# Optimization experiments

Hardware: AMD Instinct MI355X
Metric: run time of the kernel (lower is better)

Reference implementation:

```python
import jax, jax.numpy as jnp
import numpy as np
import math

B, N, H, D = 2, 2048, 16, 64

def setup_inputs() -> dict:
    key = jax.random.key(0)
    kq, kk, kv = jax.random.split(key, 3)
    q = jax.random.normal(kq, (B, N, H, D), dtype=jnp.float32)
    k = jax.random.normal(kk, (B, N, H, D), dtype=jnp.float32)
    v = jax.random.normal(kv, (B, N, H, D), dtype=jnp.float32)
    return {"q": q, "k": k, "v": v}

def reference(q, k, v):
    d = q.shape[-1]
    # [b,n,h,d] -> [b,h,n,d]
    qh = jnp.transpose(q, (0, 2, 1, 3))
    kh = jnp.transpose(k, (0, 2, 1, 3))
    vh = jnp.transpose(v, (0, 2, 1, 3))
    # scores: [b,h,n,n]
    scores = jnp.einsum('bhqd,bhkd->bhqk', qh, kh) / math.sqrt(d)
    # jax.nn.softmax performs the stable max-subtraction internally,
    # matching the original's explicit max-subtract + softmax.
    attn = jax.nn.softmax(scores, axis=-1)
    o = jnp.einsum('bhqk,bhkd->bhqd', attn, vh)
    # back to [b,n,h,d]
    return jnp.transpose(o, (0, 2, 1, 3))
```

## Files before the change

kernel.cpp:

```cpp
#include <hip/hip_runtime.h>


typedef float  f32x4  __attribute__((ext_vector_type(4)));
typedef float  f32x16 __attribute__((ext_vector_type(16)));
typedef short  s16x8  __attribute__((ext_vector_type(8)));
typedef short  s16x4  __attribute__((ext_vector_type(4)));
typedef int    i32x4  __attribute__((ext_vector_type(4)));

#define QSCALE 0.18033688011112042f

__device__ __forceinline__ unsigned short bf16r(float f) {
    unsigned u = __builtin_bit_cast(unsigned, f);
    u += 0x7fffu + ((u >> 16) & 1u);
    return (unsigned short)(u >> 16);
}

__device__ __forceinline__ s16x8 cvt8f(const float* p) {
    f32x4 a = *(const f32x4*)p;
    f32x4 b = *(const f32x4*)(p + 4);
    s16x8 r;
#pragma unroll
    for (int i = 0; i < 4; ++i) { r[i] = (short)bf16r(a[i]); r[i+4] = (short)bf16r(b[i]); }
    return r;
}

__device__ __forceinline__ s16x8 cvt8f_scaled(const float* p, float s) {
    f32x4 a = *(const f32x4*)p;
    f32x4 b = *(const f32x4*)(p + 4);
    s16x8 r;
#pragma unroll
    for (int i = 0; i < 4; ++i) {
        r[i]   = (short)bf16r(a[i] * s);
        r[i+4] = (short)bf16r(b[i] * s);
    }
    return r;
}

__device__ __forceinline__ int cvtpk2(float lo, float hi) {
    int r;
    asm("v_cvt_pk_bf16_f32 %0, %1, %2" : "=v"(r) : "v"(lo), "v"(hi));
    return r;
}

__global__ void __launch_bounds__(256)
prep(const float* __restrict__ K, const float* __restrict__ V,
     unsigned short* __restrict__ Kt, unsigned short* __restrict__ Vt) {
    const int t = threadIdx.x, bid = blockIdx.x;
    const int bh = bid & 31, nb = bid >> 5;
    const int b = bh >> 4, h = bh & 15;
    const size_t tile0 = ((size_t)bh * 64 + nb * 2) * 2048;

#pragma unroll
    for (int i = 0; i < 2; ++i) {
        const int lin = t * 2 + i;
        const int kbl = lin >> 8, rem = lin & 255;
        const int kc = rem >> 6, l = rem & 63;
        const int nl = l & 31, gg = l >> 5;
        const float* src = K + ((size_t)(b * 2048 + nb * 64 + kbl * 32 + nl)) * 1024
                             + h * 64 + kc * 16 + gg * 8;
        *(s16x8*)(Kt + tile0 + kbl * 2048 + kc * 512 + l * 8) = cvt8f(src);
    }

    __shared__ short tile[64 * 72];
    {
        const int l16 = t & 15, r = t >> 4;
#pragma unroll
        for (int p = 0; p < 4; ++p) {
            const int key = p * 16 + r;
            const float* vp = V + ((size_t)(b * 2048 + nb * 64 + key)) * 1024
                                + h * 64 + l16 * 4;
            f32x4 x = *(const f32x4*)vp;
#pragma unroll
            for (int i2 = 0; i2 < 4; ++i2)
                tile[(l16 * 4 + i2) * 72 + key] = (short)bf16r(x[i2]);
        }
    }
    __syncthreads();
#pragma unroll
    for (int i = 0; i < 2; ++i) {
        const int lin = t * 2 + i;
        const int kbl = lin >> 8, rem = lin & 255;
        const int qq = rem >> 6, l = rem & 63;
        const int dt = qq >> 1, s = qq & 1;
        const int nl = l & 31, gg = l >> 5;
        const int base = (dt * 32 + nl) * 72 + kbl * 32 + 8 * s + 4 * gg;
        s16x4 lo = *(const s16x4*)&tile[base];
        s16x4 hi = *(const s16x4*)&tile[base + 16];
        *(s16x8*)(Vt + tile0 + kbl * 2048 + qq * 512 + l * 8) =
            __builtin_shufflevector(lo, hi, 0, 1, 2, 3, 4, 5, 6, 7);
    }
}

__global__ void __launch_bounds__(256, 3)
attn_fwd(const float* __restrict__ Q, const unsigned short* __restrict__ Kt,
         const unsigned short* __restrict__ Vt, float* __restrict__ O)
{
    __shared__ __align__(16) float ex[2 * 64 * 36];

    const int t = threadIdx.x;
    const int w = t >> 6, lane = t & 63;
    const int g = lane >> 5, nl = lane & 31;
    const int qsel = w & 1, ksel = w >> 1;

    const int bid = blockIdx.x;
    const int bh  = bid & 31, qb = bid >> 5;
    const int b   = bh >> 4,  h  = bh & 15;
    const int q0  = qb * 64 + qsel * 32;

    s16x8 qf[4];
    {
        const float* qp = Q + ((size_t)(b * 2048 + q0 + nl)) * 1024 + h * 64 + g * 8;
#pragma unroll
        for (int kc = 0; kc < 4; ++kc)
            qf[kc] = cvt8f_scaled(qp + kc * 16, QSCALE);
    }

    const unsigned short* kp = Kt + (size_t)bh * 131072 + (size_t)ksel * 65536 + lane * 8;
    const unsigned short* vp = Vt + (size_t)bh * 131072 + (size_t)ksel * 65536 + lane * 8;

    f32x16 oa0 = {}, oa1 = {};
    float lp = 0.f;

    s16x8 kfa[4], vfa[4], kfb[4], vfb[4];

#define LOADT(KD, VD, IT) do {                                              \
        const unsigned short* _k = kp + (IT) * 2048;                        \
        const unsigned short* _v = vp + (IT) * 2048;                        \
        _Pragma("unroll")                                                   \
        for (int _i = 0; _i < 4; ++_i) {                                    \
            KD[_i] = *(const s16x8*)(_k + _i * 512);                        \
            VD[_i] = *(const s16x8*)(_v + _i * 512);                        \
        } } while (0)

#define STEP(KF, VF) do {                                                   \
        f32x16 sacc = {};                                                   \
        _Pragma("unroll")                                                   \
        for (int _kc = 0; _kc < 4; ++_kc)                                   \
            sacc = __builtin_amdgcn_mfma_f32_32x32x16_bf16(                 \
                KF[_kc], qf[_kc], sacc, 0, 0, 0);                           \
        float pr[16];                                                       \
        _Pragma("unroll")                                                   \
        for (int _r = 0; _r < 16; ++_r) pr[_r] = __builtin_amdgcn_exp2f(sacc[_r]); \
        _Pragma("unroll")                                                   \
        for (int _r = 0; _r < 16; ++_r) lp += pr[_r];                       \
        int pk[8];                                                          \
        _Pragma("unroll")                                                   \
        for (int _i = 0; _i < 8; ++_i) pk[_i] = cvtpk2(pr[2*_i], pr[2*_i+1]); \
        _Pragma("unroll")                                                   \
        for (int _s = 0; _s < 2; ++_s) {                                    \
            i32x4 bd = { pk[_s*2], pk[_s*2+1], pk[_s*2+4], pk[_s*2+5] };    \
            s16x8 bb = __builtin_bit_cast(s16x8, bd);                       \
            oa0 = __builtin_amdgcn_mfma_f32_32x32x16_bf16(VF[_s],     bb, oa0, 0, 0, 0); \
            oa1 = __builtin_amdgcn_mfma_f32_32x32x16_bf16(VF[2 + _s], bb, oa1, 0, 0, 0); \
        } } while (0)

    LOADT(kfa, vfa, 0);
    for (int it = 0; it < 32; it += 2) {
        LOADT(kfb, vfb, it + 1);
        STEP(kfa, vfa);
        if (it + 2 < 32) LOADT(kfa, vfa, it + 2);
        STEP(kfb, vfb);
    }
#undef LOADT
#undef STEP

    float* zone = ex + qsel * (64 * 36) + lane * 36;
    if (ksel) {
#pragma unroll
        for (int i = 0; i < 4; ++i) {
            *(f32x4*)(zone + i * 4) =
                (f32x4){ oa0[4*i], oa0[4*i+1], oa0[4*i+2], oa0[4*i+3] };
            *(f32x4*)(zone + 16 + i * 4) =
                (f32x4){ oa1[4*i], oa1[4*i+1], oa1[4*i+2], oa1[4*i+3] };
        }
        zone[32] = lp;
    }
    __syncthreads();
    if (!ksel) {
#pragma unroll
        for (int i = 0; i < 4; ++i) {
            f32x4 u0 = *(const f32x4*)(zone + i * 4);
            f32x4 u1 = *(const f32x4*)(zone + 16 + i * 4);
#pragma unroll
            for (int j = 0; j < 4; ++j) { oa0[4*i+j] += u0[j]; oa1[4*i+j] += u1[j]; }
        }
        float ssum = lp + zone[32];
        ssum += __shfl_xor(ssum, 32);
        const float inv = 1.0f / ssum;
        float* op = O + ((size_t)(b * 2048 + q0 + nl)) * 1024 + h * 64;
#pragma unroll
        for (int rq = 0; rq < 4; ++rq) {
            const int d0 = 8 * rq + 4 * g;
            *(f32x4*)(op + d0) = (f32x4){
                oa0[4*rq]   * inv, oa0[4*rq+1] * inv,
                oa0[4*rq+2] * inv, oa0[4*rq+3] * inv };
            *(f32x4*)(op + 32 + d0) = (f32x4){
                oa1[4*rq]   * inv, oa1[4*rq+1] * inv,
                oa1[4*rq+2] * inv, oa1[4*rq+3] * inv };
        }
    }
}

extern "C" void kernel_launch(void* const* d_in, const int* in_sizes, int n_in,
                              void* d_out, int out_size, void* d_ws, size_t ws_size,
                              hipStream_t stream) {
    const float* q = (const float*)d_in[0];
    const float* k = (const float*)d_in[1];
    const float* v = (const float*)d_in[2];
    float* o = (float*)d_out;

    unsigned short* Kt = (unsigned short*)d_ws;
    unsigned short* Vt = Kt + 4194304;

    hipLaunchKernelGGL(prep,     dim3(1024), dim3(256), 0, stream, k, v, Kt, Vt);
    hipLaunchKernelGGL(attn_fwd, dim3(1024), dim3(256), 0, stream, q, Kt, Vt, o);
}
```

Measured before the change: 137.0 us.

## Split keys four ways per 32-query block and drop LDS transpose in prep

The attention kernel now gives each block 32 queries and splits the key range across four waves, each covering 512 keys. Three waves write partial outputs to shared memory for the first wave to reduce, and the grid doubles to 2048 blocks. The main loop is fully unrolled with scheduling barriers, and the exp-sum is accumulated as a vector. The prep kernel drops its shared-memory V transpose in favour of strided direct global loads and packed bf16 conversion. The trade-off is more partial-sum reduction traffic, more Q reloads, and uncoalesced V reads in exchange for more parallelism and shorter per-wave dependency chains.

```diff
diff --git a/kernel.cpp b/kernel.cpp
--- a/kernel.cpp
+++ b/kernel.cpp
@@ -13,15 +13,6 @@
     unsigned u = __builtin_bit_cast(unsigned, f);
     u += 0x7fffu + ((u >> 16) & 1u);
     return (unsigned short)(u >> 16);
-}
-
-__device__ __forceinline__ s16x8 cvt8f(const float* p) {
-    f32x4 a = *(const f32x4*)p;
-    f32x4 b = *(const f32x4*)(p + 4);
-    s16x8 r;
-#pragma unroll
-    for (int i = 0; i < 4; ++i) { r[i] = (short)bf16r(a[i]); r[i+4] = (short)bf16r(b[i]); }
-    return r;
 }
 
 __device__ __forceinline__ s16x8 cvt8f_scaled(const float* p, float s) {
@@ -52,42 +43,33 @@
 
 #pragma unroll
     for (int i = 0; i < 2; ++i) {
-        const int lin = t * 2 + i;
+        const int lin = i * 256 + t;
         const int kbl = lin >> 8, rem = lin & 255;
         const int kc = rem >> 6, l = rem & 63;
         const int nl = l & 31, gg = l >> 5;
         const float* src = K + ((size_t)(b * 2048 + nb * 64 + kbl * 32 + nl)) * 1024
                              + h * 64 + kc * 16 + gg * 8;
-        *(s16x8*)(Kt + tile0 + kbl * 2048 + kc * 512 + l * 8) = cvt8f(src);
-    }
-
-    __shared__ short tile[64 * 72];
-    {
-        const int l16 = t & 15, r = t >> 4;
-#pragma unroll
-        for (int p = 0; p < 4; ++p) {
-            const int key = p * 16 + r;
-            const float* vp = V + ((size_t)(b * 2048 + nb * 64 + key)) * 1024
-                                + h * 64 + l16 * 4;
-            f32x4 x = *(const f32x4*)vp;
-#pragma unroll
-            for (int i2 = 0; i2 < 4; ++i2)
-                tile[(l16 * 4 + i2) * 72 + key] = (short)bf16r(x[i2]);
-        }
-    }
-    __syncthreads();
+        f32x4 a = *(const f32x4*)src;
+        f32x4 c = *(const f32x4*)(src + 4);
+        i32x4 o = { cvtpk2(a[0], a[1]), cvtpk2(a[2], a[3]),
+                    cvtpk2(c[0], c[1]), cvtpk2(c[2], c[3]) };
+        *(i32x4*)(Kt + tile0 + kbl * 2048 + kc * 512 + l * 8) = o;
+    }
+
 #pragma unroll
     for (int i = 0; i < 2; ++i) {
-        const int lin = t * 2 + i;
+        const int lin = i * 256 + t;
         const int kbl = lin >> 8, rem = lin & 255;
         const int qq = rem >> 6, l = rem & 63;
         const int dt = qq >> 1, s = qq & 1;
         const int nl = l & 31, gg = l >> 5;
-        const int base = (dt * 32 + nl) * 72 + kbl * 32 + 8 * s + 4 * gg;
-        s16x4 lo = *(const s16x4*)&tile[base];
-        s16x4 hi = *(const s16x4*)&tile[base + 16];
-        *(s16x8*)(Vt + tile0 + kbl * 2048 + qq * 512 + l * 8) =
-            __builtin_shufflevector(lo, hi, 0, 1, 2, 3, 4, 5, 6, 7);
+        const float* vp0 = V + ((size_t)(b * 2048 + nb * 64 + kbl * 32 + 8 * s + 4 * gg)) * 1024
+                             + h * 64 + dt * 32 + nl;
+        float x0 = vp0[0],     x1 = vp0[1024],  x2 = vp0[2048],  x3 = vp0[3072];
+        float x4 = vp0[16384], x5 = vp0[17408], x6 = vp0[18432], x7 = vp0[19456];
+        i32x4 o = { cvtpk2(x0, x1), cvtpk2(x2, x3),
+                    cvtpk2(x4, x5), cvtpk2(x6, x7) };
+        *(i32x4*)(Vt + tile0 + kbl * 2048 + qq * 512 + l * 8) = o;
     }
 }
 
@@ -95,17 +77,16 @@
 attn_fwd(const float* __restrict__ Q, const unsigned short* __restrict__ Kt,
          const unsigned short* __restrict__ Vt, float* __restrict__ O)
 {
-    __shared__ __align__(16) float ex[2 * 64 * 36];
+    __shared__ __align__(16) float ex[3 * 64 * 36];
 
     const int t = threadIdx.x;
-    const int w = t >> 6, lane = t & 63;
+    const int ksel = t >> 6, lane = t & 63;
     const int g = lane >> 5, nl = lane & 31;
-    const int qsel = w & 1, ksel = w >> 1;
 
     const int bid = blockIdx.x;
     const int bh  = bid & 31, qb = bid >> 5;
     const int b   = bh >> 4,  h  = bh & 15;
-    const int q0  = qb * 64 + qsel * 32;
+    const int q0  = qb * 32;
 
     s16x8 qf[4];
     {
@@ -115,11 +96,11 @@
             qf[kc] = cvt8f_scaled(qp + kc * 16, QSCALE);
     }
 
-    const unsigned short* kp = Kt + (size_t)bh * 131072 + (size_t)ksel * 65536 + lane * 8;
-    const unsigned short* vp = Vt + (size_t)bh * 131072 + (size_t)ksel * 65536 + lane * 8;
+    const unsigned short* kp = Kt + (size_t)bh * 131072 + (size_t)ksel * 32768 + lane * 8;
+    const unsigned short* vp = Vt + (size_t)bh * 131072 + (size_t)ksel * 32768 + lane * 8;
 
     f32x16 oa0 = {}, oa1 = {};
-    float lp = 0.f;
+    f32x4  lpv = {};
 
     s16x8 kfa[4], vfa[4], kfb[4], vfb[4];
 
@@ -138,14 +119,17 @@
         for (int _kc = 0; _kc < 4; ++_kc)                                   \
             sacc = __builtin_amdgcn_mfma_f32_32x32x16_bf16(                 \
                 KF[_kc], qf[_kc], sacc, 0, 0, 0);                           \
-        float pr[16];                                                       \
-        _Pragma("unroll")                                                   \
-        for (int _r = 0; _r < 16; ++_r) pr[_r] = __builtin_amdgcn_exp2f(sacc[_r]); \
-        _Pragma("unroll")                                                   \
-        for (int _r = 0; _r < 16; ++_r) lp += pr[_r];                       \
         int pk[8];                                                          \
         _Pragma("unroll")                                                   \
-        for (int _i = 0; _i < 8; ++_i) pk[_i] = cvtpk2(pr[2*_i], pr[2*_i+1]); \
+        for (int _c = 0; _c < 4; ++_c) {                                    \
+            f32x4 e = { __builtin_amdgcn_exp2f(sacc[4*_c]),                 \
+                        __builtin_amdgcn_exp2f(sacc[4*_c+1]),               \
+                        __builtin_amdgcn_exp2f(sacc[4*_c+2]),               \
+                        __builtin_amdgcn_exp2f(sacc[4*_c+3]) };             \
+            lpv += e;                                                       \
+            pk[2*_c]   = cvtpk2(e[0], e[1]);                                \
+            pk[2*_c+1] = cvtpk2(e[2], e[3]);                                \
+        }                                                                   \
         _Pragma("unroll")                                                   \
         for (int _s = 0; _s < 2; ++_s) {                                    \
             i32x4 bd = { pk[_s*2], pk[_s*2+1], pk[_s*2+4], pk[_s*2+5] };    \
@@ -155,17 +139,26 @@
         } } while (0)
 
     LOADT(kfa, vfa, 0);
-    for (int it = 0; it < 32; it += 2) {
-        LOADT(kfb, vfb, it + 1);
-        STEP(kfa, vfa);
-        if (it + 2 < 32) LOADT(kfa, vfa, it + 2);
-        STEP(kfb, vfb);
-    }
+    LOADT(kfb, vfb, 1);
+#pragma unroll
+    for (int it = 0; it < 16; ++it) {
+        __builtin_amdgcn_sched_barrier(0);
+        if ((it & 1) == 0) {
+            STEP(kfa, vfa);
+            if (it + 2 < 16) LOADT(kfa, vfa, it + 2);
+        } else {
+            STEP(kfb, vfb);
+            if (it + 2 < 16) LOADT(kfb, vfb, it + 2);
+        }
+    }
+    __builtin_amdgcn_sched_barrier(0);
 #undef LOADT
 #undef STEP
 
-    float* zone = ex + qsel * (64 * 36) + lane * 36;
+    const float lp = lpv[0] + lpv[1] + lpv[2] + lpv[3];
+
     if (ksel) {
+        float* zone = ex + (ksel - 1) * 2304 + lane * 36;
 #pragma unroll
         for (int i = 0; i < 4; ++i) {
             *(f32x4*)(zone + i * 4) =
@@ -177,15 +170,20 @@
     }
     __syncthreads();
     if (!ksel) {
-#pragma unroll
-        for (int i = 0; i < 4; ++i) {
-            f32x4 u0 = *(const f32x4*)(zone + i * 4);
-            f32x4 u1 = *(const f32x4*)(zone + 16 + i * 4);
-#pragma unroll
-            for (int j = 0; j < 4; ++j) { oa0[4*i+j] += u0[j]; oa1[4*i+j] += u1[j]; }
-        }
-        float ssum = lp + zone[32];
-        ssum += __shfl_xor(ssum, 32);
+        float lps = lp;
+#pragma unroll
+        for (int z = 0; z < 3; ++z) {
+            const float* zn = ex + z * 2304 + lane * 36;
+#pragma unroll
+            for (int i = 0; i < 4; ++i) {
+                f32x4 u0 = *(const f32x4*)(zn + i * 4);
+                f32x4 u1 = *(const f32x4*)(zn + 16 + i * 4);
+#pragma unroll
+                for (int j = 0; j < 4; ++j) { oa0[4*i+j] += u0[j]; oa1[4*i+j] += u1[j]; }
+            }
+            lps += zn[32];
+        }
+        float ssum = lps + __shfl_xor(lps, 32);
         const float inv = 1.0f / ssum;
         float* op = O + ((size_t)(b * 2048 + q0 + nl)) * 1024 + h * 64;
 #pragma unroll
@@ -213,5 +211,5 @@
     unsigned short* Vt = Kt + 4194304;
 
     hipLaunchKernelGGL(prep,     dim3(1024), dim3(256), 0, stream, k, v, Kt, Vt);
-    hipLaunchKernelGGL(attn_fwd, dim3(1024), dim3(256), 0, stream, q, Kt, Vt, o);
-}
+    hipLaunchKernelGGL(attn_fwd, dim3(2048), dim3(256), 0, stream, q, Kt, Vt, o);
+}
```

New measurement: 137.9 us. Within noise of the previous version (+0.7%).
